# Kernel tuning notes

Hardware: AMD Instinct MI355X
Metric: run time of the kernel (lower is better)

The kernel has to match this reference:

```python
import jax, jax.numpy as jnp
import numpy as np

LOW_T = 0.05
HIGH_T = 0.15

SOBEL_X = jnp.array([[-1., 0., 1.], [-2., 0., 2.], [-1., 0., 1.]], dtype=jnp.float32).reshape(1, 1, 3, 3)
SOBEL_Y = jnp.array([[1., 2., 1.], [0., 0., 0.], [-1., -2., -1.]], dtype=jnp.float32).reshape(1, 1, 3, 3)


def _conv3x3(x, k):
    # NCHW conv, padding=1, stride=1 (matches F.conv2d(x, k, padding=1))
    return jax.lax.conv_general_dilated(x, k, window_strides=(1, 1), padding=((1, 1), (1, 1)))


def setup_inputs() -> dict:
    key = jax.random.key(0)
    x = jax.random.normal(key, (1, 1, 4096, 4096), dtype=jnp.float32)
    return {"x": x}


def reference(x):
    grad_x = _conv3x3(x, SOBEL_X)
    grad_y = _conv3x3(x, SOBEL_Y)
    grad_mag = jnp.sqrt(grad_x * grad_x + grad_y * grad_y)
    grad_dir = jnp.arctan2(grad_y, grad_x)  # radians, as in the original (compared to degree thresholds)

    m = grad_mag[0, 0]  # [H, W]
    d = grad_dir[0, 0][1:-1, 1:-1]  # direction at interior pixels [H-2, W-2]
    H, W = m.shape

    def sh(dr, dc):
        # magnitude at (row+dr, col+dc) for interior pixels
        return m[1 + dr:H - 1 + dr, 1 + dc:W - 1 + dc]

    mc = sh(0, 0)

    # Branch predicates replicated literally from the torch code (degree thresholds
    # vs radian values; some sub-conditions are vacuously false, kept for faithfulness).
    b1 = ((d >= -22.5) & (d <= 22.5)) | ((d >= 157.5) & (d <= 180.0)) | ((d >= -157.5) & (d <= -180.0))
    b2 = ((d > 22.5) & (d <= 67.5)) | ((d >= -112.5) & (d < -157.5))
    b3 = ((d > 67.5) & (d <= 112.5)) | ((d >= -67.5) & (d < -22.5))

    mag_prev = jnp.where(b1, sh(0, -1), jnp.where(b2, sh(-1, 1), jnp.where(b3, sh(-1, 0), sh(-1, -1))))
    mag_next = jnp.where(b1, sh(0, 1), jnp.where(b2, sh(1, -1), jnp.where(b3, sh(1, 0), sh(1, 1))))

    keep = (mc >= mag_prev) & (mc >= mag_next)
    interior = jnp.where(keep, mc, jnp.zeros_like(mc))
    edges = jnp.zeros_like(m).at[1:-1, 1:-1].set(interior)

    # Double thresholding: strong -> 255, weak ([low, high]) -> 0, below-low passes through.
    strong = edges > HIGH_T
    weak = (edges >= LOW_T) & (edges <= HIGH_T)
    out = jnp.where(strong, jnp.float32(255.0), jnp.where(weak, jnp.float32(0.0), edges))
    return out  # [H, W]
```

## Files before the change

kernel.cpp:

```cpp
#include <hip/hip_runtime.h>
#include <math.h>


constexpr int Wd = 4096;
constexpr int Ht = 4096;

typedef float f4 __attribute__((ext_vector_type(4)));

__global__ __launch_bounds__(256) void canny_kernel(const float* __restrict__ x,
                                                    float* __restrict__ out) {
    const int tid   = threadIdx.x;
    const int lane  = tid & 63;
    const int r     = blockIdx.y * 4 + (tid >> 6);
    const int cbase = blockIdx.x * 1024 + lane * 16;

    const int rm = r > 0 ? r - 1 : 0;
    const int rp = r < Ht - 1 ? r + 1 : Ht - 1;

    const float* rowa = x + (size_t)rm * Wd;
    const float* rowb = x + (size_t)r  * Wd;
    const float* rowc = x + (size_t)rp * Wd;

    int off[6];
    #pragma unroll
    for (int k = 0; k < 6; ++k) {
        int c = cbase - 4 + 4 * k;
        off[k] = c < 0 ? 0 : (c > Wd - 4 ? Wd - 4 : c);
    }

    float ar[24], br[24], cr[24];
    #pragma unroll
    for (int k = 0; k < 6; ++k) {
        *(f4*)(ar + 4 * k) = *(const f4*)(rowa + off[k]);
        *(f4*)(br + 4 * k) = *(const f4*)(rowb + off[k]);
        *(f4*)(cr + 4 * k) = *(const f4*)(rowc + off[k]);
    }

    float t1[20], t2[20];
    #pragma unroll
    for (int j = 0; j < 20; ++j) {
        float a = ar[j + 2], b = br[j + 2], c = cr[j + 2];
        t1[j] = a + 2.0f * b + c;
        t2[j] = a - c;
    }

    if (blockIdx.x == 0 && lane == 0) {
        t1[0] = 0.f; t2[0] = 0.f; t1[1] = 0.f; t2[1] = 0.f;
    }
    if (blockIdx.x == 3 && lane == 63) {
        t1[18] = 0.f; t2[18] = 0.f; t1[19] = 0.f; t2[19] = 0.f;
    }

    float q[18];
    #pragma unroll
    for (int i = 0; i < 18; ++i) {
        float gx = t1[i + 2] - t1[i];
        float gy = t2[i] + 2.0f * t2[i + 1] + t2[i + 2];
        q[i] = gx * gx + gy * gy;
    }

    const float C1  = __uint_as_float(0x3CB851EDu);
    const float C2B = __uint_as_float(0x3B23D709u);

    bool hazard = false;
    #pragma unroll
    for (int i = 0; i < 17; ++i) {
        int d = (int)(__float_as_uint(q[i + 1]) - __float_as_uint(q[i]));
        hazard |= ((unsigned)(d + 8) < 17u);
    }

    float acc[16];
    #pragma unroll
    for (int o = 0; o < 16; ++o) {
        float qp = q[o], qc = q[o + 1], qn = q[o + 2];
        bool keep = (qc >= qp) && (qc >= qn);
        acc[o] = (keep && qc > C1) ? 255.0f : 0.0f;
        hazard |= (keep && qc > 0.0f && qc <= C2B);
    }

    if (__any(hazard)) {
        float m[18];
        #pragma unroll
        for (int i = 0; i < 18; ++i) m[i] = sqrtf(q[i]);
        #pragma unroll
        for (int o = 0; o < 16; ++o) {
            float mc = m[o + 1];
            bool keep = (mc >= m[o]) && (mc >= m[o + 2]);
            float e = keep ? mc : 0.0f;
            acc[o] = (e > 0.15f) ? 255.0f : ((e >= 0.05f) ? 0.0f : e);
        }
    }

    if (r == 0 || r == Ht - 1) {
        #pragma unroll
        for (int o = 0; o < 16; ++o) acc[o] = 0.0f;
    }
    if (blockIdx.x == 0 && lane == 0)  acc[0]  = 0.0f;
    if (blockIdx.x == 3 && lane == 63) acc[15] = 0.0f;

    float* op = out + (size_t)r * Wd + cbase;
    #pragma unroll
    for (int k = 0; k < 4; ++k) {
        f4 v = {acc[4 * k], acc[4 * k + 1], acc[4 * k + 2], acc[4 * k + 3]};
        *(f4*)(op + 4 * k) = v;
    }
}

extern "C" void kernel_launch(void* const* d_in, const int* in_sizes, int n_in,
                              void* d_out, int out_size, void* d_ws, size_t ws_size,
                              hipStream_t stream) {
    const float* x = (const float*)d_in[0];
    float* out = (float*)d_out;
    dim3 grid(4, 1024);
    canny_kernel<<<grid, dim3(256), 0, stream>>>(x, out);
}
```

Baseline: 130.5 us.

## Shrink per-thread work to 4 columns and share halos via lane shuffles

Each thread now processes 4 columns instead of 16, and the grid grows from 4 to 16 blocks along the width. Horizontal neighbours come from wavefront shuffles instead of redundant overlapping loads, and only edge lanes load halo vectors. This removes the duplicated halo reads and the large register arrays, raising occupancy and making loads fully coalesced, at the cost of shuffle instructions and more threads.

Measured after the change: 117.7 us. -9.8%, faster.

```diff
diff --git a/kernel.cpp b/kernel.cpp
--- a/kernel.cpp
+++ b/kernel.cpp
@@ -9,10 +9,12 @@
 
 __global__ __launch_bounds__(256) void canny_kernel(const float* __restrict__ x,
                                                     float* __restrict__ out) {
-    const int tid   = threadIdx.x;
-    const int lane  = tid & 63;
-    const int r     = blockIdx.y * 4 + (tid >> 6);
-    const int cbase = blockIdx.x * 1024 + lane * 16;
+    const int tid  = threadIdx.x;
+    const int lane = tid & 63;
+    const int r    = blockIdx.y * 4 + (tid >> 6);
+    const int wc   = blockIdx.x;
+    const int cbase = wc * 256;
+    const int c     = cbase + lane * 4;
 
     const int rm = r > 0 ? r - 1 : 0;
     const int rp = r < Ht - 1 ? r + 1 : Ht - 1;
@@ -21,41 +23,49 @@
     const float* rowb = x + (size_t)r  * Wd;
     const float* rowc = x + (size_t)rp * Wd;
 
-    int off[6];
+    f4 a  = *(const f4*)(rowa + c);
+    f4 b  = *(const f4*)(rowb + c);
+    f4 cc = *(const f4*)(rowc + c);
+
+    float t1[4], t2[4];
     #pragma unroll
-    for (int k = 0; k < 6; ++k) {
-        int c = cbase - 4 + 4 * k;
-        off[k] = c < 0 ? 0 : (c > Wd - 4 ? Wd - 4 : c);
+    for (int j = 0; j < 4; ++j) {
+        t1[j] = a[j] + 2.0f * b[j] + cc[j];
+        t2[j] = a[j] - cc[j];
     }
 
-    float ar[24], br[24], cr[24];
-    #pragma unroll
-    for (int k = 0; k < 6; ++k) {
-        *(f4*)(ar + 4 * k) = *(const f4*)(rowa + off[k]);
-        *(f4*)(br + 4 * k) = *(const f4*)(rowb + off[k]);
-        *(f4*)(cr + 4 * k) = *(const f4*)(rowc + off[k]);
+    float hl1[2] = {0.f, 0.f}, hl2[2] = {0.f, 0.f};
+    float hr1[2] = {0.f, 0.f}, hr2[2] = {0.f, 0.f};
+    if (lane == 0 && wc > 0) {
+        f4 ha = *(const f4*)(rowa + cbase - 4);
+        f4 hb = *(const f4*)(rowb + cbase - 4);
+        f4 hc = *(const f4*)(rowc + cbase - 4);
+        hl1[0] = ha[2] + 2.0f * hb[2] + hc[2];  hl2[0] = ha[2] - hc[2];
+        hl1[1] = ha[3] + 2.0f * hb[3] + hc[3];  hl2[1] = ha[3] - hc[3];
+    }
+    if (lane == 63 && wc < 15) {
+        f4 ha = *(const f4*)(rowa + cbase + 256);
+        f4 hb = *(const f4*)(rowb + cbase + 256);
+        f4 hc = *(const f4*)(rowc + cbase + 256);
+        hr1[0] = ha[0] + 2.0f * hb[0] + hc[0];  hr2[0] = ha[0] - hc[0];
+        hr1[1] = ha[1] + 2.0f * hb[1] + hc[1];  hr2[1] = ha[1] - hc[1];
     }
 
-    float t1[20], t2[20];
+    float l1a = __shfl_up(t1[2], 1),  l1b = __shfl_up(t1[3], 1);
+    float l2a = __shfl_up(t2[2], 1),  l2b = __shfl_up(t2[3], 1);
+    float r1a = __shfl_down(t1[0], 1), r1b = __shfl_down(t1[1], 1);
+    float r2a = __shfl_down(t2[0], 1), r2b = __shfl_down(t2[1], 1);
+    if (lane == 0)  { l1a = hl1[0]; l1b = hl1[1]; l2a = hl2[0]; l2b = hl2[1]; }
+    if (lane == 63) { r1a = hr1[0]; r1b = hr1[1]; r2a = hr2[0]; r2b = hr2[1]; }
+
+    float T1[8] = {l1a, l1b, t1[0], t1[1], t1[2], t1[3], r1a, r1b};
+    float T2[8] = {l2a, l2b, t2[0], t2[1], t2[2], t2[3], r2a, r2b};
+
+    float q[6];
     #pragma unroll
-    for (int j = 0; j < 20; ++j) {
-        float a = ar[j + 2], b = br[j + 2], c = cr[j + 2];
-        t1[j] = a + 2.0f * b + c;
-        t2[j] = a - c;
-    }
-
-    if (blockIdx.x == 0 && lane == 0) {
-        t1[0] = 0.f; t2[0] = 0.f; t1[1] = 0.f; t2[1] = 0.f;
-    }
-    if (blockIdx.x == 3 && lane == 63) {
-        t1[18] = 0.f; t2[18] = 0.f; t1[19] = 0.f; t2[19] = 0.f;
-    }
-
-    float q[18];
-    #pragma unroll
-    for (int i = 0; i < 18; ++i) {
-        float gx = t1[i + 2] - t1[i];
-        float gy = t2[i] + 2.0f * t2[i + 1] + t2[i + 2];
+    for (int i = 0; i < 6; ++i) {
+        float gx = T1[i + 2] - T1[i];
+        float gy = T2[i] + 2.0f * T2[i + 1] + T2[i + 2];
         q[i] = gx * gx + gy * gy;
     }
 
@@ -64,14 +74,14 @@
 
     bool hazard = false;
     #pragma unroll
-    for (int i = 0; i < 17; ++i) {
+    for (int i = 0; i < 5; ++i) {
         int d = (int)(__float_as_uint(q[i + 1]) - __float_as_uint(q[i]));
         hazard |= ((unsigned)(d + 8) < 17u);
     }
 
-    float acc[16];
+    float acc[4];
     #pragma unroll
-    for (int o = 0; o < 16; ++o) {
+    for (int o = 0; o < 4; ++o) {
         float qp = q[o], qc = q[o + 1], qn = q[o + 2];
         bool keep = (qc >= qp) && (qc >= qn);
         acc[o] = (keep && qc > C1) ? 255.0f : 0.0f;
@@ -79,11 +89,11 @@
     }
 
     if (__any(hazard)) {
-        float m[18];
+        float m[6];
         #pragma unroll
-        for (int i = 0; i < 18; ++i) m[i] = sqrtf(q[i]);
+        for (int i = 0; i < 6; ++i) m[i] = sqrtf(q[i]);
         #pragma unroll
-        for (int o = 0; o < 16; ++o) {
+        for (int o = 0; o < 4; ++o) {
             float mc = m[o + 1];
             bool keep = (mc >= m[o]) && (mc >= m[o + 2]);
             float e = keep ? mc : 0.0f;
@@ -93,17 +103,13 @@
 
     if (r == 0 || r == Ht - 1) {
         #pragma unroll
-        for (int o = 0; o < 16; ++o) acc[o] = 0.0f;
+        for (int o = 0; o < 4; ++o) acc[o] = 0.0f;
     }
-    if (blockIdx.x == 0 && lane == 0)  acc[0]  = 0.0f;
-    if (blockIdx.x == 3 && lane == 63) acc[15] = 0.0f;
+    if (wc == 0  && lane == 0)  acc[0] = 0.0f;
+    if (wc == 15 && lane == 63) acc[3] = 0.0f;
 
-    float* op = out + (size_t)r * Wd + cbase;
-    #pragma unroll
-    for (int k = 0; k < 4; ++k) {
-        f4 v = {acc[4 * k], acc[4 * k + 1], acc[4 * k + 2], acc[4 * k + 3]};
-        *(f4*)(op + 4 * k) = v;
-    }
+    f4 v = {acc[0], acc[1], acc[2], acc[3]};
+    *(f4*)(out + (size_t)r * Wd + c) = v;
 }
 
 extern "C" void kernel_launch(void* const* d_in, const int* in_sizes, int n_in,
@@ -111,6 +117,6 @@
                               hipStream_t stream) {
     const float* x = (const float*)d_in[0];
     float* out = (float*)d_out;
-    dim3 grid(4, 1024);
+    dim3 grid(16, 1024);
     canny_kernel<<<grid, dim3(256), 0, stream>>>(x, out);
 }
```
